# Kernel optimization log

Hardware: AMD Instinct MI355X
Metric: run time of the kernel (lower is better)

Reference implementation:

```python
import jax, jax.numpy as jnp
import numpy as np

# Static config (from MSDeformAttnPixelDecoder defaults, 1024x1024 input, strides 8/16/32 reversed)
SHAPES = [(32, 32), (64, 64), (128, 128)]  # (H, W) per level, order as fed to the transformer
B, C, NH, NL, NP, NLAYERS, DFF = 4, 256, 8, 3, 4, 6, 1024
HD = C // NH
S = sum(h * w for h, w in SHAPES)
STARTS = np.concatenate([[0], np.cumsum([h * w for h, w in SHAPES])[:-1]]).tolist()


def setup_inputs() -> dict:
    key = jax.random.key(0)
    ks = jax.random.split(key, 24)
    def nrm(k, shape, scale):
        return jax.random.normal(k, shape, jnp.float32) * scale
    inp = {}
    for i, (h, w) in enumerate(SHAPES):
        inp[f'src{i}'] = jax.random.normal(ks[i], (B, C, h, w), jnp.float32)
        inp[f'pos{i}'] = jax.random.normal(ks[3 + i], (B, C, h, w), jnp.float32)
    L = NLAYERS
    inp['level_embed'] = nrm(ks[6], (NL, C), 1.0)
    inp['Wv'] = nrm(ks[7], (L, C, C), 0.02); inp['bv'] = jnp.zeros((L, C), jnp.float32)
    inp['Wo'] = nrm(ks[8], (L, C, NH * NL * NP * 2), 0.01)
    inp['bo'] = nrm(ks[9], (L, NH * NL * NP * 2), 0.5)  # stands in for the grid-init offset bias
    inp['Wa'] = nrm(ks[10], (L, C, NH * NL * NP), 0.02); inp['ba'] = jnp.zeros((L, NH * NL * NP), jnp.float32)
    inp['Wout'] = nrm(ks[11], (L, C, C), 0.02); inp['bout'] = jnp.zeros((L, C), jnp.float32)
    inp['ln1_g'] = jnp.ones((L, C), jnp.float32); inp['ln1_b'] = jnp.zeros((L, C), jnp.float32)
    inp['W1'] = nrm(ks[12], (L, C, DFF), 0.02); inp['b1'] = jnp.zeros((L, DFF), jnp.float32)
    inp['W2'] = nrm(ks[13], (L, DFF, C), 0.02); inp['b2'] = jnp.zeros((L, C), jnp.float32)
    inp['ln2_g'] = jnp.ones((L, C), jnp.float32); inp['ln2_b'] = jnp.zeros((L, C), jnp.float32)
    return inp


def _layer_norm(x, g, b):
    m = x.mean(-1, keepdims=True)
    v = ((x - m) ** 2).mean(-1, keepdims=True)
    return (x - m) * jax.lax.rsqrt(v + 1e-5) * g + b


def _bilinear_sample(v, loc):
    # v: [BH, Hl, Wl, D]; loc: [BH, P, 2] normalized (x, y) in [0,1].
    # Matches F.grid_sample(mode=bilinear, padding_mode=zeros, align_corners=False)
    BH, Hl, Wl, D = v.shape
    x = loc[..., 0] * Wl - 0.5
    y = loc[..., 1] * Hl - 0.5
    x0f = jnp.floor(x); y0f = jnp.floor(y)
    lx = x - x0f; ly = y - y0f
    x0 = x0f.astype(jnp.int32); y0 = y0f.astype(jnp.int32)
    bidx = jnp.arange(BH)[:, None]
    def g(yi, xi):
        valid = (xi >= 0) & (xi < Wl) & (yi >= 0) & (yi < Hl)
        vi = v[bidx, jnp.clip(yi, 0, Hl - 1), jnp.clip(xi, 0, Wl - 1)]
        return jnp.where(valid[..., None], vi, 0.0)
    v00 = g(y0, x0); v01 = g(y0, x0 + 1); v10 = g(y0 + 1, x0); v11 = g(y0 + 1, x0 + 1)
    wx0 = 1.0 - lx; wy0 = 1.0 - ly
    return (v00 * (wx0 * wy0)[..., None] + v01 * (lx * wy0)[..., None]
            + v10 * (wx0 * ly)[..., None] + v11 * (lx * ly)[..., None])


def _forward(src0, src1, src2, pos0, pos1, pos2, level_embed,
             Wv, bv, Wo, bo, Wa, ba, Wout, bout, ln1_g, ln1_b,
             W1, b1, W2, b2, ln2_g, ln2_b):
    srcs, poss = [src0, src1, src2], [pos0, pos1, pos2]
    # Flatten [B,C,H,W] -> [B,HW,C], add level embedding to pos
    src = jnp.concatenate([s.reshape(B, C, -1).transpose(0, 2, 1) for s in srcs], axis=1)
    pos = jnp.concatenate([
        p.reshape(B, C, -1).transpose(0, 2, 1) + level_embed[i][None, None, :]
        for i, p in enumerate(poss)], axis=1)
    # Reference points: pixel centers, normalized; valid_ratios == 1 (masks all False)
    refs = []
    for h, w in SHAPES:
        ry = (jnp.arange(h, dtype=jnp.float32) + 0.5) / h
        rx = (jnp.arange(w, dtype=jnp.float32) + 0.5) / w
        gy, gx = jnp.meshgrid(ry, rx, indexing='ij')
        refs.append(jnp.stack([gx.reshape(-1), gy.reshape(-1)], -1))
    ref = jnp.concatenate(refs, 0)  # [S, 2] (x, y); same for every level since valid_ratios=1
    wh = jnp.array([[w, h] for h, w in SHAPES], jnp.float32)  # [NL, 2] (W, H)

    output = src
    for l in range(NLAYERS):
        q = output + pos
        value = (output @ Wv[l] + bv[l]).reshape(B, S, NH, HD)
        offs = (q @ Wo[l] + bo[l]).reshape(B, S, NH, NL, NP, 2)
        aw = jax.nn.softmax((q @ Wa[l] + ba[l]).reshape(B, S, NH, NL * NP), axis=-1)
        aw = aw.reshape(B, S, NH, NL, NP)
        loc = ref[None, :, None, None, None, :] + offs / wh[None, None, None, :, None, :]
        attn = jnp.zeros((B, S, NH, HD), output.dtype)
        for lvl, (h, w) in enumerate(SHAPES):
            s0 = STARTS[lvl]
            v_l = value[:, s0:s0 + h * w].transpose(0, 2, 1, 3).reshape(B * NH, h, w, HD)
            loc_l = loc[:, :, :, lvl].transpose(0, 2, 1, 3, 4).reshape(B * NH, S * NP, 2)
            samp = _bilinear_sample(v_l, loc_l).reshape(B, NH, S, NP, HD)
            attn = attn + jnp.einsum('bhspd,bshp->bshd', samp, aw[:, :, :, lvl])
        attn_out = attn.reshape(B, S, C) @ Wout[l] + bout[l]
        output = _layer_norm(output + attn_out, ln1_g[l], ln1_b[l])
        ff = jax.nn.relu(output @ W1[l] + b1[l]) @ W2[l] + b2[l]
        output = _layer_norm(output + ff, ln2_g[l], ln2_b[l])
    return output  # [B, S, C] encoder memory


def reference(src0, src1, src2, pos0, pos1, pos2, level_embed,
              Wv, bv, Wo, bo, Wa, ba, Wout, bout, ln1_g, ln1_b,
              W1, b1, W2, b2, ln2_g, ln2_b):
    return _forward(src0, src1, src2, pos0, pos1, pos2, level_embed,
                    Wv, bv, Wo, bo, Wa, ba, Wout, bout, ln1_g, ln1_b,
                    W1, b1, W2, b2, ln2_g, ln2_b)
```

## Files before the change

kernel.cpp:

```cpp
#include <hip/hip_runtime.h>
#include <hip/hip_fp16.h>
#include <stdint.h>

#define S_TOT 21504
#define M_TOK 86016

typedef __attribute__((ext_vector_type(8))) short bf16x8;
typedef __attribute__((ext_vector_type(4))) float f32x4;
typedef __attribute__((ext_vector_type(2))) float f32x2;

__device__ __forceinline__ unsigned short f2b(float f) {
  union { float f; unsigned u; } v; v.f = f;
  unsigned r = v.u + 0x7FFFu + ((v.u >> 16) & 1u);
  return (unsigned short)(r >> 16);
}
__device__ __forceinline__ unsigned short f2h(float f) {
  __half h = __float2half(f);
  return __half_as_ushort(h);
}
__device__ __forceinline__ float b2f(unsigned short h) {
  union { unsigned u; float f; } v; v.u = ((unsigned)h) << 16;
  return v.f;
}
__device__ __forceinline__ float blo(unsigned u) {
  union { unsigned u; float f; } v; v.u = u << 16; return v.f;
}
__device__ __forceinline__ float bhi(unsigned u) {
  union { unsigned u; float f; } v; v.u = u & 0xffff0000u; return v.f;
}
__device__ __forceinline__ float h2lo(unsigned u) {
  union { unsigned u; __half2 h; } v; v.u = u; return __half2float(v.h.x);
}
__device__ __forceinline__ float h2hi(unsigned u) {
  union { unsigned u; __half2 h; } v; v.u = u; return __half2float(v.h.y);
}

#define LSTR 40
template <int RELU, int OUTH>
__global__ __launch_bounds__(256) void gemm_kernel(
    const unsigned short* __restrict__ A, const unsigned short* __restrict__ Bt,
    const float* __restrict__ bias, const float* __restrict__ bias2, int nsplit,
    unsigned short* __restrict__ C, int N, int K, int ntx) {
  __shared__ unsigned short Alds[128 * LSTR];
  __shared__ unsigned short Blds[128 * LSTR];
  const int tid = threadIdx.x;
  const int wave = tid >> 6, lane = tid & 63;
  const int nblk = gridDim.x, chunk = nblk >> 3;
  const int bid = blockIdx.x;
  const int swz = (bid & 7) * chunk + (bid >> 3);
  const long m0 = (long)(swz / ntx) * 128;
  const int n0 = (swz % ntx) * 128;
  const int wm = (wave >> 1) * 64, wn = (wave & 1) * 64;

  f32x4 acc[4][4];
#pragma unroll
  for (int i = 0; i < 4; i++)
#pragma unroll
    for (int j = 0; j < 4; j++) acc[i][j] = (f32x4){0.f, 0.f, 0.f, 0.f};

  const int ar = tid >> 2, ak = (tid & 3) * 8;
  int brA = n0 + ar;      if (brA >= N) brA = N - 1;
  int brB = n0 + ar + 64; if (brB >= N) brB = N - 1;
  const unsigned short* a0p = A + (m0 + ar) * (long)K + ak;
  const unsigned short* a1p = A + (m0 + ar + 64) * (long)K + ak;
  const unsigned short* b0p = Bt + (long)brA * K + ak;
  const unsigned short* b1p = Bt + (long)brB * K + ak;
  unsigned short* aw0 = Alds + ar * LSTR + ak;
  unsigned short* aw1 = Alds + (ar + 64) * LSTR + ak;
  unsigned short* bw0 = Blds + ar * LSTR + ak;
  unsigned short* bw1 = Blds + (ar + 64) * LSTR + ak;

  uint4 a0 = *(const uint4*)a0p;
  uint4 a1 = *(const uint4*)a1p;
  uint4 b0 = *(const uint4*)b0p;
  uint4 b1 = *(const uint4*)b1p;

  for (int k0 = 0; k0 < K; k0 += 32) {
    if (k0) __syncthreads();
    *(uint4*)aw0 = a0;
    *(uint4*)aw1 = a1;
    *(uint4*)bw0 = b0;
    *(uint4*)bw1 = b1;
    if (k0 + 32 < K) {
      a0 = *(const uint4*)(a0p + k0 + 32);
      a1 = *(const uint4*)(a1p + k0 + 32);
      b0 = *(const uint4*)(b0p + k0 + 32);
      b1 = *(const uint4*)(b1p + k0 + 32);
    }
    __syncthreads();

    const int kk = (lane >> 4) * 8;
    bf16x8 af[4], bq[4];
#pragma unroll
    for (int i = 0; i < 4; i++)
      af[i] = *(const bf16x8*)&Alds[(wm + i * 16 + (lane & 15)) * LSTR + kk];
#pragma unroll
    for (int j = 0; j < 4; j++)
      bq[j] = *(const bf16x8*)&Blds[(wn + j * 16 + (lane & 15)) * LSTR + kk];
#pragma unroll
    for (int i = 0; i < 4; i++)
#pragma unroll
      for (int j = 0; j < 4; j++)
        acc[i][j] = __builtin_amdgcn_mfma_f32_16x16x32_bf16(af[i], bq[j], acc[i][j], 0, 0, 0);
  }

  unsigned short* stage = Alds;
  const int colb = lane & 15, rowb = (lane >> 4) * 4;
#pragma unroll
  for (int half = 0; half < 2; half++) {
    __syncthreads();
    if (wm == half * 64) {
#pragma unroll
      for (int j = 0; j < 4; j++) {
        const int n = n0 + wn + j * 16 + colb;
        const float bn = (n < N) ? ((n < nsplit) ? bias[n] : bias2[n - nsplit]) : 0.f;
#pragma unroll
        for (int i = 0; i < 4; i++) {
#pragma unroll
          for (int r = 0; r < 4; r++) {
            float v = acc[i][j][r] + bn;
            if (RELU) v = fmaxf(v, 0.f);
            stage[(i * 16 + rowb + r) * 136 + wn + j * 16 + colb] = OUTH ? f2h(v) : f2b(v);
          }
        }
      }
    }
    __syncthreads();
#pragma unroll
    for (int t = 0; t < 4; t++) {
      const int idx = t * 256 + tid;
      const int rr = idx >> 4;
      const int cc = (idx & 15) * 8;
      const int n = n0 + cc;
      if (n < N) {
        const long m = m0 + half * 64 + rr;
        *(uint4*)(C + m * N + n) = *(const uint4*)(stage + rr * 136 + cc);
      }
    }
  }
}

__global__ void wtrans_kernel(const float* __restrict__ src, unsigned short* __restrict__ dst,
                              int K, int N, size_t src_lstride, size_t dst_lstride) {
  __shared__ float t[32][33];
  const int tx = threadIdx.x, ty = threadIdx.y;
  const int n0 = blockIdx.x * 32, k0 = blockIdx.y * 32, l = blockIdx.z;
  src += (size_t)l * src_lstride;
  dst += (size_t)l * dst_lstride;
#pragma unroll
  for (int i = 0; i < 4; i++) t[ty * 4 + i][tx] = src[(size_t)(k0 + ty * 4 + i) * N + n0 + tx];
  __syncthreads();
#pragma unroll
  for (int i = 0; i < 4; i++)
    dst[(size_t)(n0 + ty * 4 + i) * K + k0 + tx] = f2b(t[tx][ty * 4 + i]);
}

__global__ void flatten_kernel(const float* __restrict__ src, const float* __restrict__ pos,
                               const float* __restrict__ lemb,
                               unsigned short* __restrict__ outb, unsigned short* __restrict__ posb,
                               unsigned short* __restrict__ qb, int HW, int s0) {
  __shared__ float ts[32][33];
  __shared__ float tp[32][33];
  const int tx = threadIdx.x, ty = threadIdx.y;
  const int hw0 = blockIdx.x * 32, c0 = blockIdx.y * 32, b = blockIdx.z;
  const size_t ibase = ((size_t)b * 256 + c0) * HW + hw0;
#pragma unroll
  for (int i = 0; i < 4; i++) {
    ts[ty * 4 + i][tx] = src[ibase + (size_t)(ty * 4 + i) * HW + tx];
    tp[ty * 4 + i][tx] = pos[ibase + (size_t)(ty * 4 + i) * HW + tx];
  }
  __syncthreads();
#pragma unroll
  for (int i = 0; i < 4; i++) {
    const int sI = s0 + hw0 + ty * 4 + i, c = c0 + tx;
    const size_t o = ((size_t)b * S_TOT + sI) * 256 + c;
    const float sv = ts[tx][ty * 4 + i];
    const unsigned short pb = f2b(tp[tx][ty * 4 + i] + lemb[c]);
    outb[o] = f2b(sv);
    posb[o] = pb;
    qb[o] = f2b(sv + b2f(pb));
  }
}

__global__ __launch_bounds__(256) void deform_kernel(const unsigned short* __restrict__ value,
                                                     const unsigned short* __restrict__ oa,
                                                     unsigned short* __restrict__ attn) {
  __shared__ float law[4][96];
  __shared__ uint4 didx[4][96];
  __shared__ float4 dwt[4][96];
  const int tid = threadIdx.x;
  const int wv = tid >> 6, lane = tid & 63;
  const int bs = blockIdx.x * 4 + wv;
  const int b = bs / S_TOT, s = bs - b * S_TOT;

  if (lane < 8) {
    const unsigned short* ap = oa + (size_t)bs * 288 + 192 + lane * 12;
    const uint2 p0 = *(const uint2*)ap;
    const uint2 p1 = *(const uint2*)(ap + 4);
    const uint2 p2 = *(const uint2*)(ap + 8);
    float a[12] = {blo(p0.x), bhi(p0.x), blo(p0.y), bhi(p0.y),
                   blo(p1.x), bhi(p1.x), blo(p1.y), bhi(p1.y),
                   blo(p2.x), bhi(p2.x), blo(p2.y), bhi(p2.y)};
    float mx = a[0];
#pragma unroll
    for (int i = 1; i < 12; i++) mx = fmaxf(mx, a[i]);
    float e[12], sm = 0.f;
#pragma unroll
    for (int i = 0; i < 12; i++) { e[i] = __expf(a[i] - mx); sm += e[i]; }
    const float r = 1.f / sm;
#pragma unroll
    for (int i = 0; i < 12; i++) law[wv][lane * 12 + i] = e[i] * r;
  }
  __syncthreads();

  float rx, ry;
  {
    if (s < 1024) { const int li = s; rx = ((li & 31) + 0.5f) * (1.f / 32); ry = ((li >> 5) + 0.5f) * (1.f / 32); }
    else if (s < 5120) { const int li = s - 1024; rx = ((li & 63) + 0.5f) * (1.f / 64); ry = ((li >> 6) + 0.5f) * (1.f / 64); }
    else { const int li = s - 5120; rx = ((li & 127) + 0.5f) * (1.f / 128); ry = ((li >> 7) + 0.5f) * (1.f / 128); }
  }

  for (int ti = lane; ti < 96; ti += 64) {
    const int h = ti / 12;
    const int rem = ti - h * 12;
    const int lvl = rem >> 2;
    const int wl = 32 << lvl;
    const float fwl = (float)wl;
    const int start = (lvl == 0) ? 0 : ((lvl == 1) ? 1024 : 5120);
    const unsigned op = *(const unsigned*)(oa + (size_t)bs * 288 + 2 * ti);
    const float ox = blo(op), oy = bhi(op);
    const float x = (rx + ox / fwl) * fwl - 0.5f;
    const float y = (ry + oy / fwl) * fwl - 0.5f;
    const float xf = floorf(x), yf = floorf(y);
    const int x0 = (int)xf, y0 = (int)yf;
    const float fx = x - xf, fy = y - yf;
    const bool xv0 = (x0 >= 0) & (x0 < wl), xv1 = (x0 + 1 >= 0) & (x0 + 1 < wl);
    const bool yv0 = (y0 >= 0) & (y0 < wl), yv1 = (y0 + 1 >= 0) & (y0 + 1 < wl);
    const int x0c = min(max(x0, 0), wl - 1), x1c = min(max(x0 + 1, 0), wl - 1);
    const int y0c = min(max(y0, 0), wl - 1), y1c = min(max(y0 + 1, 0), wl - 1);
    const float w = law[wv][ti];
    float4 w4;
    w4.x = (xv0 & yv0) ? w * (1.f - fx) * (1.f - fy) : 0.f;
    w4.y = (xv1 & yv0) ? w * fx * (1.f - fy) : 0.f;
    w4.z = (xv0 & yv1) ? w * (1.f - fx) * fy : 0.f;
    w4.w = (xv1 & yv1) ? w * fx * fy : 0.f;
    const unsigned base = (unsigned)(((b * S_TOT + start) << 8) + h * 32) * 2u;
    uint4 iv;
    iv.x = base + (unsigned)(y0c * wl + x0c) * 512u;
    iv.y = base + (unsigned)(y0c * wl + x1c) * 512u;
    iv.z = base + (unsigned)(y1c * wl + x0c) * 512u;
    iv.w = base + (unsigned)(y1c * wl + x1c) * 512u;
    didx[wv][ti] = iv;
    dwt[wv][ti] = w4;
  }
  __syncthreads();

  const int h = lane >> 3, c = (lane & 7) * 4;
  const char* vb = (const char*)value + c * 2;
  const uint4* ip = &didx[wv][h * 12];
  const float4* wp = &dwt[wv][h * 12];
  float a0 = 0.f, a1 = 0.f, a2 = 0.f, a3 = 0.f;
#pragma unroll
  for (int t = 0; t < 12; t++) {
    const uint4 iv = ip[t];
    const float4 w4 = wp[t];
    const uint2 q00 = *(const uint2*)(vb + iv.x);
    const uint2 q01 = *(const uint2*)(vb + iv.y);
    const uint2 q10 = *(const uint2*)(vb + iv.z);
    const uint2 q11 = *(const uint2*)(vb + iv.w);
    a0 += w4.x * h2lo(q00.x); a1 += w4.x * h2hi(q00.x);
    a2 += w4.x * h2lo(q00.y); a3 += w4.x * h2hi(q00.y);
    a0 += w4.y * h2lo(q01.x); a1 += w4.y * h2hi(q01.x);
    a2 += w4.y * h2lo(q01.y); a3 += w4.y * h2hi(q01.y);
    a0 += w4.z * h2lo(q10.x); a1 += w4.z * h2hi(q10.x);
    a2 += w4.z * h2lo(q10.y); a3 += w4.z * h2hi(q10.y);
    a0 += w4.w * h2lo(q11.x); a1 += w4.w * h2hi(q11.x);
    a2 += w4.w * h2lo(q11.y); a3 += w4.w * h2hi(q11.y);
  }
  uint2 o;
  o.x = (unsigned)f2b(a0) | ((unsigned)f2b(a1) << 16);
  o.y = (unsigned)f2b(a2) | ((unsigned)f2b(a3) << 16);
  *(uint2*)(attn + (size_t)bs * 256 + h * 32 + c) = o;
}

__global__ __launch_bounds__(256) void resln_kernel(const unsigned short* __restrict__ x,
                                                    const unsigned short* __restrict__ r,
                                                    const float* __restrict__ g,
                                                    const float* __restrict__ bta,
                                                    unsigned short* __restrict__ ob,
                                                    const unsigned short* __restrict__ pos,
                                                    unsigned short* __restrict__ qb,
                                                    float* __restrict__ fout) {
  const int t = blockIdx.x * 4 + (threadIdx.x >> 6);
  const int lane = threadIdx.x & 63;
  const size_t base = (size_t)t * 256;
  const ushort4 xv = ((const ushort4*)(x + base))[lane];
  const ushort4 rv = ((const ushort4*)(r + base))[lane];
  const float v0 = b2f(xv.x) + b2f(rv.x), v1 = b2f(xv.y) + b2f(rv.y);
  const float v2 = b2f(xv.z) + b2f(rv.z), v3 = b2f(xv.w) + b2f(rv.w);
  float sm = v0 + v1 + v2 + v3;
#pragma unroll
  for (int o = 32; o > 0; o >>= 1) sm += __shfl_xor(sm, o);
  const float mean = sm * (1.f / 256.f);
  const float d0 = v0 - mean, d1 = v1 - mean, d2 = v2 - mean, d3 = v3 - mean;
  float vs = d0 * d0 + d1 * d1 + d2 * d2 + d3 * d3;
#pragma unroll
  for (int o = 32; o > 0; o >>= 1) vs += __shfl_xor(vs, o);
  const float inv = rsqrtf(vs * (1.f / 256.f) + 1e-5f);
  const int c = lane * 4;
  const float o0 = d0 * inv * g[c] + bta[c];
  const float o1 = d1 * inv * g[c + 1] + bta[c + 1];
  const float o2 = d2 * inv * g[c + 2] + bta[c + 2];
  const float o3 = d3 * inv * g[c + 3] + bta[c + 3];
  if (fout) {
    ((float4*)(fout + base))[lane] = make_float4(o0, o1, o2, o3);
  } else {
    ushort4 u;
    u.x = f2b(o0); u.y = f2b(o1); u.z = f2b(o2); u.w = f2b(o3);
    ((ushort4*)(ob + base))[lane] = u;
  }
  if (qb) {
    const ushort4 pv = ((const ushort4*)(pos + base))[lane];
    ushort4 u;
    u.x = f2b(o0 + b2f(pv.x)); u.y = f2b(o1 + b2f(pv.y));
    u.z = f2b(o2 + b2f(pv.z)); u.w = f2b(o3 + b2f(pv.w));
    ((ushort4*)(qb + base))[lane] = u;
  }
}

extern "C" void kernel_launch(void* const* d_in, const int* in_sizes, int n_in,
                              void* d_out, int out_size, void* d_ws, size_t ws_size,
                              hipStream_t stream) {
  (void)in_sizes; (void)n_in; (void)out_size;
  const float* src0 = (const float*)d_in[0];
  const float* pos0 = (const float*)d_in[1];
  const float* src1 = (const float*)d_in[2];
  const float* pos1 = (const float*)d_in[3];
  const float* src2 = (const float*)d_in[4];
  const float* pos2 = (const float*)d_in[5];
  const float* lemb = (const float*)d_in[6];
  const float* Wv = (const float*)d_in[7];   const float* bv = (const float*)d_in[8];
  const float* Wo = (const float*)d_in[9];   const float* bo = (const float*)d_in[10];
  const float* Wa = (const float*)d_in[11];  const float* ba = (const float*)d_in[12];
  const float* Wout = (const float*)d_in[13]; const float* bout = (const float*)d_in[14];
  const float* ln1g = (const float*)d_in[15]; const float* ln1b = (const float*)d_in[16];
  const float* W1 = (const float*)d_in[17];  const float* b1 = (const float*)d_in[18];
  const float* W2 = (const float*)d_in[19];  const float* b2 = (const float*)d_in[20];
  const float* ln2g = (const float*)d_in[21]; const float* ln2b = (const float*)d_in[22];

  const size_t M = M_TOK;
  const size_t SZ16 = 44040192ull;
  const size_t POOL = 176160768ull;
  const size_t NEED = SZ16 + POOL + SZ16 + SZ16 + 8749056ull;
  if (ws_size < NEED) return;

  char* ws = (char*)d_ws;
  unsigned short* slot0b = (unsigned short*)ws;
  unsigned short* valb = slot0b;
  unsigned short* woutb = slot0b;
  unsigned short* ffb = slot0b;
  char* pool = ws + SZ16;
  unsigned short* q_b16 = (unsigned short*)pool;
  unsigned short* oa_b16 = (unsigned short*)pool + M * 256;
  unsigned short* attn_b16 = (unsigned short*)pool + M * 544;
  unsigned short* h_b16 = (unsigned short*)pool;
  unsigned short* out_b16 = (unsigned short*)(pool + POOL);
  unsigned short* pos_b16 = out_b16 + M * 256;
  unsigned short* wt = pos_b16 + M * 256;

  unsigned short* wtv = wt;
  unsigned short* wtoa = wt + 393216;
  unsigned short* wtw = wt + 835584;
  unsigned short* wt1 = wt + 1228800;
  unsigned short* wt2 = wt + 2801664;

  const dim3 b32(32, 8);
  wtrans_kernel<<<dim3(8, 8, 6), b32, 0, stream>>>(Wv, wtv, 256, 256, 65536, 65536);
  wtrans_kernel<<<dim3(6, 8, 6), b32, 0, stream>>>(Wo, wtoa, 256, 192, 49152, 73728);
  wtrans_kernel<<<dim3(3, 8, 6), b32, 0, stream>>>(Wa, wtoa + 192 * 256, 256, 96, 24576, 73728);
  wtrans_kernel<<<dim3(8, 8, 6), b32, 0, stream>>>(Wout, wtw, 256, 256, 65536, 65536);
  wtrans_kernel<<<dim3(32, 8, 6), b32, 0, stream>>>(W1, wt1, 256, 1024, 262144, 262144);
  wtrans_kernel<<<dim3(8, 32, 6), b32, 0, stream>>>(W2, wt2, 1024, 256, 262144, 262144);

  flatten_kernel<<<dim3(32, 8, 4), b32, 0, stream>>>(src0, pos0, lemb, out_b16, pos_b16, q_b16, 1024, 0);
  flatten_kernel<<<dim3(128, 8, 4), b32, 0, stream>>>(src1, pos1, lemb + 256, out_b16, pos_b16, q_b16, 4096, 1024);
  flatten_kernel<<<dim3(512, 8, 4), b32, 0, stream>>>(src2, pos2, lemb + 512, out_b16, pos_b16, q_b16, 16384, 5120);

  for (int l = 0; l < 6; l++) {
    gemm_kernel<0, 1><<<1344, 256, 0, stream>>>(out_b16, wtv + l * 65536, bv + l * 256, bv + l * 256, 256, valb, 256, 256, 2);
    gemm_kernel<0, 0><<<2016, 256, 0, stream>>>(q_b16, wtoa + l * 73728, bo + l * 192, ba + l * 96, 192, oa_b16, 288, 256, 3);
    deform_kernel<<<21504, 256, 0, stream>>>(valb, oa_b16, attn_b16);
    gemm_kernel<0, 0><<<1344, 256, 0, stream>>>(attn_b16, wtw + l * 65536, bout + l * 256, bout + l * 256, 256, woutb, 256, 256, 2);
    resln_kernel<<<21504, 256, 0, stream>>>(out_b16, woutb, ln1g + l * 256, ln1b + l * 256, out_b16, nullptr, nullptr, nullptr);
    gemm_kernel<1, 0><<<5376, 256, 0, stream>>>(out_b16, wt1 + l * 262144, b1 + l * 1024, b1 + l * 1024, 1024, h_b16, 1024, 256, 8);
    gemm_kernel<0, 0><<<1344, 256, 0, stream>>>(h_b16, wt2 + l * 262144, b2 + l * 256, b2 + l * 256, 256, ffb, 256, 1024, 2);
    if (l < 5) {
      resln_kernel<<<21504, 256, 0, stream>>>(out_b16, ffb, ln2g + l * 256, ln2b + l * 256, out_b16, pos_b16, q_b16, nullptr);
    } else {
      resln_kernel<<<21504, 256, 0, stream>>>(out_b16, ffb, ln2g + l * 256, ln2b + l * 256, nullptr, nullptr, nullptr, (float*)d_out);
    }
  }
}
```

Measured before the change: 2.657 ms.

## Double-buffer GEMM LDS tiles and drop per-wave block barriers in sampler

The GEMM kernel now uses two LDS buffers for the A and B tiles and processes two K-steps per loop iteration. The next tile is written into the alternate buffer while the current one is being consumed, so each K-step needs one barrier instead of two. The deformable-attention sampling kernel drops two __syncthreads that guarded per-wave LDS arrays, relying on intra-wave ordering instead. This doubles GEMM LDS use, which may lower occupancy. Removing the barriers risks races if the compiler reorders the LDS accesses within a wave.

```diff
diff --git a/kernel.cpp b/kernel.cpp
--- a/kernel.cpp
+++ b/kernel.cpp
@@ -36,13 +36,13 @@
 }
 
 #define LSTR 40
+#define TSZ (128 * LSTR)
 template <int RELU, int OUTH>
 __global__ __launch_bounds__(256) void gemm_kernel(
     const unsigned short* __restrict__ A, const unsigned short* __restrict__ Bt,
     const float* __restrict__ bias, const float* __restrict__ bias2, int nsplit,
     unsigned short* __restrict__ C, int N, int K, int ntx) {
-  __shared__ unsigned short Alds[128 * LSTR];
-  __shared__ unsigned short Blds[128 * LSTR];
+  __shared__ unsigned short smem[4 * TSZ];
   const int tid = threadIdx.x;
   const int wave = tid >> 6, lane = tid & 63;
   const int nblk = gridDim.x, chunk = nblk >> 3;
@@ -65,46 +65,73 @@
   const unsigned short* a1p = A + (m0 + ar + 64) * (long)K + ak;
   const unsigned short* b0p = Bt + (long)brA * K + ak;
   const unsigned short* b1p = Bt + (long)brB * K + ak;
-  unsigned short* aw0 = Alds + ar * LSTR + ak;
-  unsigned short* aw1 = Alds + (ar + 64) * LSTR + ak;
-  unsigned short* bw0 = Blds + ar * LSTR + ak;
-  unsigned short* bw1 = Blds + (ar + 64) * LSTR + ak;
-
-  uint4 a0 = *(const uint4*)a0p;
-  uint4 a1 = *(const uint4*)a1p;
-  uint4 b0 = *(const uint4*)b0p;
-  uint4 b1 = *(const uint4*)b1p;
-
-  for (int k0 = 0; k0 < K; k0 += 32) {
-    if (k0) __syncthreads();
-    *(uint4*)aw0 = a0;
-    *(uint4*)aw1 = a1;
-    *(uint4*)bw0 = b0;
-    *(uint4*)bw1 = b1;
+  const int wo0 = ar * LSTR + ak, wo1 = (ar + 64) * LSTR + ak;
+
+  uint4 ra0 = *(const uint4*)a0p;
+  uint4 ra1 = *(const uint4*)a1p;
+  uint4 rb0 = *(const uint4*)b0p;
+  uint4 rb1 = *(const uint4*)b1p;
+  *(uint4*)(smem + wo0) = ra0;
+  *(uint4*)(smem + wo1) = ra1;
+  *(uint4*)(smem + 2 * TSZ + wo0) = rb0;
+  *(uint4*)(smem + 2 * TSZ + wo1) = rb1;
+  if (32 < K) {
+    ra0 = *(const uint4*)(a0p + 32);
+    ra1 = *(const uint4*)(a1p + 32);
+    rb0 = *(const uint4*)(b0p + 32);
+    rb1 = *(const uint4*)(b1p + 32);
+  }
+  __syncthreads();
+
+#define GEMM_COMPUTE(P)                                                               \
+  {                                                                                   \
+    const int kk = (lane >> 4) * 8;                                                   \
+    const unsigned short* Ab = smem + (P)*TSZ;                                        \
+    const unsigned short* Bb = smem + (2 + (P)) * TSZ;                                \
+    bf16x8 af[4], bq[4];                                                              \
+    _Pragma("unroll") for (int i = 0; i < 4; i++)                                     \
+        af[i] = *(const bf16x8*)&Ab[(wm + i * 16 + (lane & 15)) * LSTR + kk];         \
+    _Pragma("unroll") for (int j = 0; j < 4; j++)                                     \
+        bq[j] = *(const bf16x8*)&Bb[(wn + j * 16 + (lane & 15)) * LSTR + kk];         \
+    _Pragma("unroll") for (int i = 0; i < 4; i++)                                     \
+        _Pragma("unroll") for (int j = 0; j < 4; j++)                                 \
+            acc[i][j] = __builtin_amdgcn_mfma_f32_16x16x32_bf16(af[i], bq[j],         \
+                                                                acc[i][j], 0, 0, 0); \
+  }
+
+  for (int k0 = 0; k0 < K; k0 += 64) {
     if (k0 + 32 < K) {
-      a0 = *(const uint4*)(a0p + k0 + 32);
-      a1 = *(const uint4*)(a1p + k0 + 32);
-      b0 = *(const uint4*)(b0p + k0 + 32);
-      b1 = *(const uint4*)(b1p + k0 + 32);
+      *(uint4*)(smem + TSZ + wo0) = ra0;
+      *(uint4*)(smem + TSZ + wo1) = ra1;
+      *(uint4*)(smem + 3 * TSZ + wo0) = rb0;
+      *(uint4*)(smem + 3 * TSZ + wo1) = rb1;
+      if (k0 + 64 < K) {
+        ra0 = *(const uint4*)(a0p + k0 + 64);
+        ra1 = *(const uint4*)(a1p + k0 + 64);
+        rb0 = *(const uint4*)(b0p + k0 + 64);
+        rb1 = *(const uint4*)(b1p + k0 + 64);
+      }
     }
+    GEMM_COMPUTE(0);
     __syncthreads();
-
-    const int kk = (lane >> 4) * 8;
-    bf16x8 af[4], bq[4];
-#pragma unroll
-    for (int i = 0; i < 4; i++)
-      af[i] = *(const bf16x8*)&Alds[(wm + i * 16 + (lane & 15)) * LSTR + kk];
-#pragma unroll
-    for (int j = 0; j < 4; j++)
-      bq[j] = *(const bf16x8*)&Blds[(wn + j * 16 + (lane & 15)) * LSTR + kk];
-#pragma unroll
-    for (int i = 0; i < 4; i++)
-#pragma unroll
-      for (int j = 0; j < 4; j++)
-        acc[i][j] = __builtin_amdgcn_mfma_f32_16x16x32_bf16(af[i], bq[j], acc[i][j], 0, 0, 0);
-  }
-
-  unsigned short* stage = Alds;
+    if (k0 + 64 < K) {
+      *(uint4*)(smem + wo0) = ra0;
+      *(uint4*)(smem + wo1) = ra1;
+      *(uint4*)(smem + 2 * TSZ + wo0) = rb0;
+      *(uint4*)(smem + 2 * TSZ + wo1) = rb1;
+      if (k0 + 96 < K) {
+        ra0 = *(const uint4*)(a0p + k0 + 96);
+        ra1 = *(const uint4*)(a1p + k0 + 96);
+        rb0 = *(const uint4*)(b0p + k0 + 96);
+        rb1 = *(const uint4*)(b1p + k0 + 96);
+      }
+    }
+    GEMM_COMPUTE(1);
+    __syncthreads();
+  }
+#undef GEMM_COMPUTE
+
+  unsigned short* stage = smem;
   const int colb = lane & 15, rowb = (lane >> 4) * 4;
 #pragma unroll
   for (int half = 0; half < 2; half++) {
@@ -211,7 +238,6 @@
 #pragma unroll
     for (int i = 0; i < 12; i++) law[wv][lane * 12 + i] = e[i] * r;
   }
-  __syncthreads();
 
   float rx, ry;
   {
@@ -253,7 +279,6 @@
     didx[wv][ti] = iv;
     dwt[wv][ti] = w4;
   }
-  __syncthreads();
 
   const int h = lane >> 3, c = (lane & 7) * 4;
   const char* vb = (const char*)value + c * 2;
```

New measurement: 2.640 ms. About the same (-0.7%).
